# Optimization experiments

Measured on AMD Instinct MI355X. Metric: run time of the kernel, lower is better.

## Reference

```python
import jax, jax.numpy as jnp
import numpy as np

DIM = 256      # block dim
NH = 4         # num_head
HD = DIM // 2  # head_dim = dim // 2 (per CrossBlock -> CroA)
HALF = DIM // 2  # channels per axial branch
DI = NH * HD   # inner qkv dim = 512
B, H, W = 8, 56, 56


def _conv1x1(w, b, x):
    # 1x1 conv == per-pixel channel matmul; w:[Cout,Cin], x:[B,Cin,H,W]
    return jnp.einsum('oc,bchw->bohw', w, x) + b[None, :, None, None]


def _mha(x, qw, qb, kw, kb, vw, vb, pw, pb, rel):
    # axial MHA over the last (W) axis, per row, matching torch MHA exactly
    Bx, C, Hx, Wx = x.shape
    q = _conv1x1(qw, qb, x).transpose(0, 2, 1, 3).reshape(Bx, Hx, NH, HD, Wx)
    k = _conv1x1(kw, kb, x).transpose(0, 2, 1, 3).reshape(Bx, Hx, NH, HD, Wx)
    v = _conv1x1(vw, vb, x).transpose(0, 2, 1, 3).reshape(Bx, Hx, NH, HD, Wx)
    att = jnp.einsum('bhndi,bhndj->bhnij', q, k) * (HD ** -0.5)
    L = Wx
    # gathered relative-position bias (RelPos); torch does this under no_grad
    idx = (jnp.arange(L)[:, None] - jnp.arange(L)[None, :] + L - 1).reshape(-1)
    bias = jax.lax.stop_gradient(rel[:, idx].reshape(NH, L, L))
    att = jax.nn.softmax(att + bias[None, None], axis=-1)
    out = jnp.einsum('bhnij,bhndj->bhnid', att, v)  # [B,H,nh,W,hd]
    # faithful to torch: raw reshape of [B*H, nh, W, hd] -> (B, H, W, nh*hd)
    out = out.reshape(Bx, Hx, Wx, NH * HD).transpose(0, 3, 1, 2)
    return _conv1x1(pw, pb, out) + x


def _forward(x, xq_w, xq_b, xk_w, xk_b, xv_w, xv_b, xp_w, xp_b, rel_x,
             yq_w, yq_b, yk_w, yk_b, yv_w, yv_b, yp_w, yp_b, rel_y,
             cp_w, cp_b, m1_w, m1_b, m2_w, m2_b, ls1, ls2):
    ax, ay = jnp.split(x, 2, axis=1)
    ax = _mha(ax, xq_w, xq_b, xk_w, xk_b, xv_w, xv_b, xp_w, xp_b, rel_x)
    ay = _mha(ay.transpose(0, 1, 3, 2), yq_w, yq_b, yk_w, yk_b, yv_w, yv_b,
              yp_w, yp_b, rel_y).transpose(0, 1, 3, 2)
    net = _conv1x1(cp_w, cp_b, jnp.concatenate([ax, ay], axis=1))
    net = net * ls1[None] + x                      # layer_scale1 + residual
    h = jax.nn.gelu(_conv1x1(m1_w, m1_b, net), approximate=False)
    out = _conv1x1(m2_w, m2_b, h)
    return out * ls2[None] + net                   # layer_scale2 + identity skip (dim==out_dim)


def setup_inputs() -> dict:
    key = jax.random.key(0)
    ks = iter(jax.random.split(key, 32))
    def w(shape, s=0.05):
        return jax.random.normal(next(ks), shape, dtype=jnp.float32) * s
    return dict(
        x=jax.random.normal(next(ks), (B, DIM, H, W), dtype=jnp.float32),
        xq_w=w((DI, HALF)), xq_b=w((DI,)), xk_w=w((DI, HALF)), xk_b=w((DI,)),
        xv_w=w((DI, HALF)), xv_b=w((DI,)), xp_w=w((HALF, DI)), xp_b=w((HALF,)),
        rel_x=jax.random.normal(next(ks), (NH, W * W), dtype=jnp.float32),
        yq_w=w((DI, HALF)), yq_b=w((DI,)), yk_w=w((DI, HALF)), yk_b=w((DI,)),
        yv_w=w((DI, HALF)), yv_b=w((DI,)), yp_w=w((HALF, DI)), yp_b=w((HALF,)),
        rel_y=jax.random.normal(next(ks), (NH, H * H), dtype=jnp.float32),
        cp_w=w((DIM, DIM)), cp_b=w((DIM,)),
        m1_w=w((2 * DIM, DIM)), m1_b=w((2 * DIM,)),
        m2_w=w((DIM, 2 * DIM)), m2_b=w((DIM,)),
        ls1=jnp.ones((DIM, 1, 1), jnp.float32),
        ls2=jnp.ones((DIM, 1, 1), jnp.float32),
    )


def reference(x, xq_w, xq_b, xk_w, xk_b, xv_w, xv_b, xp_w, xp_b, rel_x,
              yq_w, yq_b, yk_w, yk_b, yv_w, yv_b, yp_w, yp_b, rel_y,
              cp_w, cp_b, m1_w, m1_b, m2_w, m2_b, ls1, ls2):
    return _forward(x, xq_w, xq_b, xk_w, xk_b, xv_w, xv_b, xp_w, xp_b, rel_x,
                    yq_w, yq_b, yk_w, yk_b, yv_w, yv_b, yp_w, yp_b, rel_y,
                    cp_w, cp_b, m1_w, m1_b, m2_w, m2_b, ls1, ls2)
```

## Files before the change

kernel.cpp:

```cpp
#include <hip/hip_runtime.h>

using u16 = unsigned short;
using u32 = unsigned int;

typedef short bf16x8 __attribute__((ext_vector_type(8)));
typedef float f32x4 __attribute__((ext_vector_type(4)));

#define HW 3136
#define IMG 56

__device__ __forceinline__ float bf2f(u16 v) {
    union { u32 u; float f; } c; c.u = ((u32)v) << 16; return c.f;
}
__device__ __forceinline__ u16 f2bf(float f) {
    union { float f; u32 u; } c; c.f = f;
    return (u16)((c.u + 0x7fffu + ((c.u >> 16) & 1u)) >> 16);
}
__device__ __forceinline__ u32 pk2bf(float a, float b) {
    u32 r;
    asm("v_cvt_pk_bf16_f32 %0, %1, %2" : "=v"(r) : "v"(a), "v"(b));
    return r;
}
__device__ __forceinline__ int swz8(int r) { return (r ^ (r >> 3)) & 7; }

__device__ __forceinline__ f32x4 mfma16(bf16x8 a, bf16x8 b, f32x4 c) {
    return __builtin_amdgcn_mfma_f32_16x16x32_bf16(a, b, c, 0, 0, 0);
}

__device__ __forceinline__ void gl_lds(const void* g, void* l) {
    __builtin_amdgcn_global_load_lds((const __attribute__((address_space(1))) void*)g,
                                     (__attribute__((address_space(3))) void*)l, 16, 0, 0);
}

__global__ __launch_bounds__(256) void prep(
    const float* __restrict__ x, u16* __restrict__ Xt,
    const float* __restrict__ s0, const float* __restrict__ s1, const float* __restrict__ s2,
    const float* __restrict__ s3, const float* __restrict__ s4, const float* __restrict__ s5,
    const float* __restrict__ s6, const float* __restrict__ s7, const float* __restrict__ s8,
    const float* __restrict__ s9, const float* __restrict__ s10,
    const float* __restrict__ b0, const float* __restrict__ b1, const float* __restrict__ b2,
    const float* __restrict__ b3, const float* __restrict__ b4, const float* __restrict__ b5,
    const float* __restrict__ b6, const float* __restrict__ b7, const float* __restrict__ b8,
    const float* __restrict__ b9, const float* __restrict__ b10,
    u16* __restrict__ Wb, float* __restrict__ Bc)
{
    __shared__ u16 lds[64][80];
    const int t = threadIdx.x;
    const int idx = blockIdx.x;

    if (idx < 1568) {
        const int Pb = (idx % 49) * 64;
        const int Cb = ((idx / 49) & 3) * 64;
        const int b  = idx / 196;
        #pragma unroll
        for (int q = 0; q < 4; ++q) {
            int id = t + q * 256;
            int c = id >> 4, pf = (id & 15) * 4;
            float4 v = *(const float4*)(x + ((long)(b * 256 + Cb + c)) * HW + Pb + pf);
            u16 vv[4] = { f2bf(v.x), f2bf(v.y), f2bf(v.z), f2bf(v.w) };
            #pragma unroll
            for (int j = 0; j < 4; ++j) {
                int p = pf + j;
                int cc = (((c >> 3) ^ ((p >> 2) & 7)) << 3) + (c & 7);
                lds[p][cc] = vv[j];
            }
        }
        __syncthreads();
        int p = t >> 2, cf = (t & 3) * 16;
        u16* dst = Xt + ((long)b * HW + Pb + p) * 256 + Cb + cf;
        int cc0 = ((cf >> 3) + 0) ^ ((p >> 2) & 7);
        int cc1 = ((cf >> 3) + 1) ^ ((p >> 2) & 7);
        *(uint4*)(dst + 0) = *(uint4*)&lds[p][cc0 * 8];
        *(uint4*)(dst + 8) = *(uint4*)&lds[p][cc1 * 8];
        return;
    }

    const int bx = idx - 1568;
    if (bx == 832) {
        for (int i = t; i < 4352; i += 256) {
            const float* src; int off;
            if      (i < 512)  { src = b0;  off = i; }
            else if (i < 1024) { src = b1;  off = i - 512; }
            else if (i < 1536) { src = b2;  off = i - 1024; }
            else if (i < 2048) { src = b3;  off = i - 1536; }
            else if (i < 2560) { src = b4;  off = i - 2048; }
            else if (i < 3072) { src = b5;  off = i - 2560; }
            else if (i < 3200) { src = b6;  off = i - 3072; }
            else if (i < 3328) { src = b7;  off = i - 3200; }
            else if (i < 3584) { src = b8;  off = i - 3328; }
            else if (i < 4096) { src = b9;  off = i - 3584; }
            else               { src = b10; off = i - 4096; }
            Bc[i] = src[off];
        }
        return;
    }
    long gid4 = ((long)bx * 256 + t) * 4;
    const float* src; long off;
    if (gid4 < 589824) {
        int seg = (int)(gid4 >> 16);
        const float* tab[9] = { s0, s1, s2, s3, s4, s5, s6, s7, s8 };
        src = tab[seg]; off = gid4 - ((long)seg << 16);
    } else if (gid4 < 720896) { src = s9;  off = gid4 - 589824; }
    else                      { src = s10; off = gid4 - 720896; }
    float4 v = *(const float4*)(src + off);
    *(uint2*)(Wb + gid4) = make_uint2(pk2bf(v.x, v.y), pk2bf(v.z, v.w));
}

__global__ __launch_bounds__(256, 2) void fused_attn(
    const u16* __restrict__ Wb, const float* __restrict__ Bc,
    const u16* __restrict__ Xt,
    const float* __restrict__ rel_x, const float* __restrict__ rel_y,
    u16* __restrict__ SbX, u16* __restrict__ SbY)
{
    __shared__ __align__(16) char smem[66048];
    const int tid = threadIdx.x;
    const int lane = tid & 63, wid = tid >> 6;
    const int l15 = lane & 15, lg = lane >> 4;

    const int g = blockIdx.x;
    const int n = blockIdx.y;
    const int branch = blockIdx.z >> 3;
    const int b = blockIdx.z & 7;

    const float* rel = branch ? rel_y : rel_x;
    u16* S = branch ? SbY : SbX;
    const u16* wsrc = Wb + branch * 196608 + n * 16384;
    const float* bsrc = Bc + branch * 1536 + n * 128;

    if (tid < 128) {
        float v = (tid < 112) ? rel[n * HW + tid] : 0.0f;
        *(float*)(smem + 65536 + tid * 4) = v;
    }

    bf16x8 wf[3][2][4];
    #pragma unroll
    for (int mat = 0; mat < 3; ++mat)
        #pragma unroll
        for (int mt = 0; mt < 2; ++mt) {
            int mrow = (wid * 2 + mt) * 16 + l15;
            const u16* wr = wsrc + mat * 65536 + mrow * 128;
            #pragma unroll
            for (int ks = 0; ks < 4; ++ks)
                wf[mat][mt][ks] = *(const bf16x8*)(wr + (ks * 4 + lg) * 8);
        }
    float4 bq4[2], bk4[2]; float bvv[2];
    #pragma unroll
    for (int mt = 0; mt < 2; ++mt) {
        int m0 = (wid * 2 + mt) * 16 + lg * 4;
        bq4[mt] = *(const float4*)(bsrc + m0);
        bk4[mt] = *(const float4*)(bsrc + 512 + m0);
        bvv[mt] = bsrc[1024 + (wid * 2 + mt) * 16 + l15];
    }

    const int istrip = wid * 16;
    const float qscale = 0.08838834764831845f;

    auto stageX = [&](int rc2) {
        const int i0 = wid * 16 + (lane >> 4);
        #pragma unroll
        for (int t = 0; t < 4; ++t) {
            int i = i0 + t * 4;
            int ic = (i > 55) ? 55 : i;
            long p = (branch == 0) ? (long)rc2 * IMG + ic : (long)ic * IMG + rc2;
            const u16* src = Xt + ((long)b * HW + p) * 256 + branch * 128
                             + (((lane & 15) ^ swz8(i)) * 8);
            gl_lds(src, smem + 49152 + wid * 4096 + t * 1024);
        }
    };

    stageX(g * 7);

    for (int r = 0; r < 7; ++r) {
        const int rc = g * 7 + r;

        __syncthreads();

        bf16x8 xf[4][4];
        #pragma unroll
        for (int it = 0; it < 4; ++it) {
            int i = it * 16 + l15;
            #pragma unroll
            for (int ks = 0; ks < 4; ++ks)
                xf[it][ks] = *(const bf16x8*)(smem + 49152 + i * 256
                                              + (((ks * 4 + lg) ^ swz8(i)) * 16));
        }

        __builtin_amdgcn_s_setprio(1);
        #pragma unroll
        for (int mat = 0; mat < 2; ++mat) {
            #pragma unroll
            for (int mt = 0; mt < 2; ++mt) {
                #pragma unroll
                for (int it = 0; it < 4; ++it) {
                    f32x4 a = {};
                    #pragma unroll
                    for (int ks = 0; ks < 4; ++ks)
                        a = mfma16(wf[mat][mt][ks], xf[it][ks], a);
                    int i = it * 16 + l15;
                    int m0 = (wid * 2 + mt) * 16 + lg * 4;
                    float4 bb2 = mat ? bk4[mt] : bq4[mt];
                    int c = m0 >> 3;
                    *(uint2*)(smem + mat * 16384 + i * 256 + ((c ^ swz8(i)) * 16) + (lg & 1) * 8)
                        = make_uint2(pk2bf(a[0] + bb2.x, a[1] + bb2.y),
                                     pk2bf(a[2] + bb2.z, a[3] + bb2.w));
                }
            }
        }
        #pragma unroll
        for (int mt = 0; mt < 2; ++mt) {
            #pragma unroll
            for (int it = 0; it < 4; ++it) {
                f32x4 a = {};
                #pragma unroll
                for (int ks = 0; ks < 4; ++ks)
                    a = mfma16(xf[it][ks], wf[2][mt][ks], a);
                int d = (wid * 2 + mt) * 16 + l15;
                int c2 = (it >> 1) * 4 + lg;
                float bv = bvv[mt];
                *(uint2*)(smem + 32768 + d * 128 + ((c2 ^ swz8(d)) * 16) + (it & 1) * 8)
                    = make_uint2(pk2bf(a[0] + bv, a[1] + bv),
                                 pk2bf(a[2] + bv, a[3] + bv));
            }
        }
        __builtin_amdgcn_s_setprio(0);
        __syncthreads();

        if (r < 6) stageX(rc + 1);

        bf16x8 aq[4];
        #pragma unroll
        for (int ks = 0; ks < 4; ++ks) {
            int row = istrip + l15;
            int ch = ks * 4 + lg;
            aq[ks] = *(const bf16x8*)(smem + row * 256 + ((ch ^ swz8(row)) * 16));
        }
        __builtin_amdgcn_s_setprio(1);
        f32x4 sacc[4] = {};
        #pragma unroll
        for (int ct = 0; ct < 4; ++ct) {
            #pragma unroll
            for (int ks = 0; ks < 4; ++ks) {
                int j = ct * 16 + l15;
                int ch = ks * 4 + lg;
                bf16x8 kb = *(const bf16x8*)(smem + 16384 + j * 256 + ((ch ^ swz8(j)) * 16));
                sacc[ct] = mfma16(kb, aq[ks], sacc[ct]);
            }
        }
        __builtin_amdgcn_s_setprio(0);

        const int irow = istrip + l15;
        float p[4][4];
        float mx = -1e30f;
        #pragma unroll
        for (int ct = 0; ct < 4; ++ct)
            #pragma unroll
            for (int rr = 0; rr < 4; ++rr) {
                int j = ct * 16 + lg * 4 + rr;
                float x = sacc[ct][rr] * qscale;
                if (j < IMG) x += *(const float*)(smem + 65536 + (irow - j + 55) * 4);
                else x = -1e30f;
                p[ct][rr] = x;
                mx = fmaxf(mx, x);
            }
        mx = fmaxf(mx, __shfl_xor(mx, 16));
        mx = fmaxf(mx, __shfl_xor(mx, 32));
        float s0 = 0.f;
        #pragma unroll
        for (int ct = 0; ct < 4; ++ct)
            #pragma unroll
            for (int rr = 0; rr < 4; ++rr) {
                float e = __expf(p[ct][rr] - mx);
                p[ct][rr] = e; s0 += e;
            }
        s0 += __shfl_xor(s0, 16);
        s0 += __shfl_xor(s0, 32);
        float inv = 1.0f / s0;

        union { u32 u[4]; bf16x8 v; } pb[2];
        #pragma unroll
        for (int ks = 0; ks < 2; ++ks) {
            pb[ks].u[0] = pk2bf(p[2*ks][0] * inv, p[2*ks][1] * inv);
            pb[ks].u[1] = pk2bf(p[2*ks][2] * inv, p[2*ks][3] * inv);
            pb[ks].u[2] = pk2bf(p[2*ks+1][0] * inv, p[2*ks+1][1] * inv);
            pb[ks].u[3] = pk2bf(p[2*ks+1][2] * inv, p[2*ks+1][3] * inv);
        }

        __builtin_amdgcn_s_setprio(1);
        f32x4 oacc[8] = {};
        #pragma unroll
        for (int dt = 0; dt < 8; ++dt) {
            #pragma unroll
            for (int ks = 0; ks < 2; ++ks) {
                int d = dt * 16 + l15;
                int c2 = ks * 4 + lg;
                bf16x8 vb = *(const bf16x8*)(smem + 32768 + d * 128 + ((c2 ^ swz8(d)) * 16));
                oacc[dt] = mfma16(vb, pb[ks].v, oacc[dt]);
            }
        }
        __builtin_amdgcn_s_setprio(0);

        const int i = istrip + l15;
        if (i < IMG) {
            int im = n * 14 + (i >> 2);
            long pp = (branch == 0) ? (long)rc * IMG + im : (long)im * IMG + rc;
            u16* dst = S + ((long)b * HW + pp) * 512 + (i & 3) * 128;
            #pragma unroll
            for (int dt = 0; dt < 8; ++dt) {
                int d4 = dt * 16 + lg * 4;
                *(uint2*)(dst + d4) = make_uint2(pk2bf(oacc[dt][0], oacc[dt][1]),
                                                 pk2bf(oacc[dt][2], oacc[dt][3]));
            }
        }
    }
}

__global__ __launch_bounds__(256, 2) void tail(
    const u16* __restrict__ Wb, const float* __restrict__ Bc,
    const u16* __restrict__ SbX, const u16* __restrict__ SbY,
    const u16* __restrict__ Xt,
    const float* __restrict__ ls1, const float* __restrict__ ls2,
    float* __restrict__ y)
{
    __shared__ __align__(16) char smem[81920];
    const int tid = threadIdx.x;
    const int lane = tid & 63, wid = tid >> 6;
    const int l15 = lane & 15, lg = lane >> 4;
    const int P0 = blockIdx.x * 64;
    const int b  = blockIdx.z;

    const u16* xp  = Wb + 393216;
    const u16* yp  = Wb + 458752;
    const u16* cpw = Wb + 524288;
    const u16* m1w = Wb + 589824;
    const u16* m2w = Wb + 720896;

    f32x4 acc[4][4] = {};
    for (int ko = 0; ko < 512; ko += 64) {
        #pragma unroll
        for (int t = 0; t < 2; ++t) {
            int row = wid * 16 + t * 8 + (lane >> 3);
            int c = (lane & 7) ^ swz8(row);
            long prow = (long)b * HW + P0 + row;
            gl_lds(SbX + prow * 512 + ko + c * 8, smem + wid * 2048 + t * 1024);
            gl_lds(SbY + prow * 512 + ko + c * 8, smem + 8192 + wid * 2048 + t * 1024);
        }
        #pragma unroll
        for (int t = 0; t < 4; ++t) {
            int row = wid * 32 + t * 8 + (lane >> 3);
            int c = (lane & 7) ^ swz8(row);
            gl_lds(xp + (long)row * 512 + ko + c * 8, smem + 16384 + wid * 4096 + t * 1024);
            gl_lds(yp + (long)row * 512 + ko + c * 8, smem + 32768 + wid * 4096 + t * 1024);
        }
        __syncthreads();

        const int actb = (wid < 2) ? 0 : 8192;
        const int wbse = (wid < 2) ? 16384 : 32768;
        const int wrow0 = (wid & 1) * 64;
        #pragma unroll
        for (int ks = 0; ks < 2; ++ks) {
            int ch = ks * 4 + lg;
            bf16x8 af[4], bfr[4];
            #pragma unroll
            for (int rt = 0; rt < 4; ++rt) {
                int row = rt * 16 + l15;
                af[rt] = *(const bf16x8*)(smem + actb + row * 128 + ((ch ^ swz8(row)) * 16));
            }
            #pragma unroll
            for (int ct = 0; ct < 4; ++ct) {
                int row = wrow0 + ct * 16 + l15;
                bfr[ct] = *(const bf16x8*)(smem + wbse + row * 128 + ((ch ^ swz8(row)) * 16));
            }
            #pragma unroll
            for (int rt = 0; rt < 4; ++rt)
                #pragma unroll
                for (int ct = 0; ct < 4; ++ct)
                    acc[rt][ct] = mfma16(bfr[ct], af[rt], acc[rt][ct]);
        }
        __syncthreads();
    }

    #pragma unroll
    for (int rt = 0; rt < 4; ++rt) {
        int pl = rt * 16 + l15;
        long rowp = (long)b * HW + P0 + pl;
        #pragma unroll
        for (int ct = 0; ct < 4; ++ct) {
            int mg2 = wid * 64 + ct * 16 + lg * 4;
            float4 bv = *(const float4*)(Bc + 3072 + mg2);
            ushort4 rv = *(const ushort4*)(Xt + rowp * 256 + mg2);
            float v0 = acc[rt][ct][0] + bv.x + bf2f(rv.x);
            float v1 = acc[rt][ct][1] + bv.y + bf2f(rv.y);
            float v2 = acc[rt][ct][2] + bv.z + bf2f(rv.z);
            float v3 = acc[rt][ct][3] + bv.w + bf2f(rv.w);
            int cc = mg2 >> 3;
            int pos = (cc & 24) | ((cc ^ swz8(pl)) & 7);
            *(uint2*)(smem + 49152 + pl * 512 + pos * 16 + (mg2 & 7) * 2)
                = make_uint2(pk2bf(v0, v1), pk2bf(v2, v3));
        }
    }
    __syncthreads();

    f32x4 acc2[4][4] = {};
    for (int ko = 0; ko < 256; ko += 64) {
        #pragma unroll
        for (int t = 0; t < 8; ++t) {
            int row = wid * 64 + t * 8 + (lane >> 3);
            int c = (lane & 7) ^ swz8(row);
            gl_lds(cpw + (long)row * 256 + ko + c * 8, smem + 16384 + wid * 8192 + t * 1024);
        }
        __syncthreads();

        #pragma unroll
        for (int ks = 0; ks < 2; ++ks) {
            int ch = ks * 4 + lg;
            bf16x8 af[4], bfr[4];
            #pragma unroll
            for (int rt = 0; rt < 4; ++rt) {
                int row = rt * 16 + l15;
                int c = (ko >> 3) + ch;
                int pos = (c & 24) | ((c ^ swz8(row)) & 7);
                af[rt] = *(const bf16x8*)(smem + 49152 + row * 512 + pos * 16);
            }
            #pragma unroll
            for (int ct = 0; ct < 4; ++ct) {
                int row = wid * 64 + ct * 16 + l15;
                bfr[ct] = *(const bf16x8*)(smem + 16384 + row * 128 + ((ch ^ swz8(row)) * 16));
            }
            #pragma unroll
            for (int rt = 0; rt < 4; ++rt)
                #pragma unroll
                for (int ct = 0; ct < 4; ++ct)
                    acc2[rt][ct] = mfma16(bfr[ct], af[rt], acc2[rt][ct]);
        }
        __syncthreads();
    }

    #pragma unroll
    for (int rt = 0; rt < 4; ++rt) {
        int pl = rt * 16 + l15;
        long rowp = (long)b * HW + P0 + pl;
        #pragma unroll
        for (int ct = 0; ct < 4; ++ct) {
            int mg = wid * 64 + ct * 16 + lg * 4;
            float4 bv = *(const float4*)(Bc + 3328 + mg);
            float4 sv = *(const float4*)(ls1 + mg);
            ushort4 rv = *(const ushort4*)(Xt + rowp * 256 + mg);
            float v0 = (acc2[rt][ct][0] + bv.x) * sv.x + bf2f(rv.x);
            float v1 = (acc2[rt][ct][1] + bv.y) * sv.y + bf2f(rv.y);
            float v2 = (acc2[rt][ct][2] + bv.z) * sv.z + bf2f(rv.z);
            float v3 = (acc2[rt][ct][3] + bv.w) * sv.w + bf2f(rv.w);
            int cc = mg >> 3;
            int pos = (cc & 24) | ((cc ^ swz8(pl)) & 7);
            *(uint2*)(smem + 16384 + pl * 512 + pos * 16 + (mg & 7) * 2)
                = make_uint2(pk2bf(v0, v1), pk2bf(v2, v3));
        }
    }

    f32x4 aco[4][4] = {};

    for (int hc = 0; hc < 4; ++hc) {
        f32x4 ach[4][2] = {};
        for (int ko = 0; ko < 256; ko += 64) {
            #pragma unroll
            for (int t = 0; t < 4; ++t) {
                int row = wid * 32 + t * 8 + (lane >> 3);
                int c = (lane & 7) ^ swz8(row);
                gl_lds(m1w + (long)(hc * 128 + row) * 256 + ko + c * 8,
                       smem + wid * 4096 + t * 1024);
            }
            __syncthreads();

            #pragma unroll
            for (int ks = 0; ks < 2; ++ks) {
                int ch = ks * 4 + lg;
                bf16x8 af[4], bfrh[2];
                #pragma unroll
                for (int rt = 0; rt < 4; ++rt) {
                    int row = rt * 16 + l15;
                    int c = (ko >> 3) + ch;
                    int pos = (c & 24) | ((c ^ swz8(row)) & 7);
                    af[rt] = *(const bf16x8*)(smem + 16384 + row * 512 + pos * 16);
                }
                #pragma unroll
                for (int mt = 0; mt < 2; ++mt) {
                    int row = wid * 32 + mt * 16 + l15;
                    bfrh[mt] = *(const bf16x8*)(smem + row * 128 + ((ch ^ swz8(row)) * 16));
                }
                #pragma unroll
                for (int rt = 0; rt < 4; ++rt)
                    #pragma unroll
                    for (int mt = 0; mt < 2; ++mt)
                        ach[rt][mt] = mfma16(bfrh[mt], af[rt], ach[rt][mt]);
            }
            __syncthreads();
        }
        #pragma unroll
        for (int rt = 0; rt < 4; ++rt) {
            int pl = rt * 16 + l15;
            #pragma unroll
            for (int mt = 0; mt < 2; ++mt) {
                int hloc = wid * 32 + mt * 16 + lg * 4;
                float4 bv = *(const float4*)(Bc + 3584 + hc * 128 + hloc);
                float v[4];
                #pragma unroll
                for (int j = 0; j < 4; ++j) {
                    float tt = ach[rt][mt][j] + ((const float*)&bv)[j];
                    v[j] = tt * 0.5f * (1.0f + erff(tt * 0.70710678118f));
                }
                int cc = hloc >> 3;
                int pos = (cc & 8) | ((cc ^ swz8(pl)) & 7);
                *(uint2*)(smem + 49152 + pl * 256 + pos * 16 + (hloc & 7) * 2)
                    = make_uint2(pk2bf(v[0], v[1]), pk2bf(v[2], v[3]));
            }
        }

        for (int ko = 0; ko < 128; ko += 64) {
            #pragma unroll
            for (int t = 0; t < 8; ++t) {
                int row = wid * 64 + t * 8 + (lane >> 3);
                int c = (lane & 7) ^ swz8(row);
                char* dst = ((wid < 2) ? (smem + wid * 8192) : (smem + 65536 + (wid - 2) * 8192))
                            + t * 1024;
                gl_lds(m2w + (long)row * 512 + hc * 128 + ko + c * 8, dst);
            }
            __syncthreads();

            #pragma unroll
            for (int ks = 0; ks < 2; ++ks) {
                int ch = ks * 4 + lg;
                bf16x8 af[4], bfr[4];
                #pragma unroll
                for (int rt = 0; rt < 4; ++rt) {
                    int row = rt * 16 + l15;
                    int c = (ko >> 3) + ch;
                    int pos = (c & 8) | ((c ^ swz8(row)) & 7);
                    af[rt] = *(const bf16x8*)(smem + 49152 + row * 256 + pos * 16);
                }
                #pragma unroll
                for (int ct = 0; ct < 4; ++ct) {
                    int row = wid * 64 + ct * 16 + l15;
                    const char* base = (wid < 2) ? smem : (smem + 65536 - 16384);
                    bfr[ct] = *(const bf16x8*)(base + row * 128 + ((ch ^ swz8(row)) * 16));
                }
                #pragma unroll
                for (int rt = 0; rt < 4; ++rt)
                    #pragma unroll
                    for (int ct = 0; ct < 4; ++ct)
                        aco[rt][ct] = mfma16(bfr[ct], af[rt], aco[rt][ct]);
            }
            __syncthreads();
        }
    }

    #pragma unroll
    for (int rt = 0; rt < 4; ++rt) {
        int pl = rt * 16 + l15;
        #pragma unroll
        for (int ct = 0; ct < 4; ++ct) {
            int mg = wid * 64 + ct * 16 + lg * 4;
            float4 bv = *(const float4*)(Bc + 4096 + mg);
            float4 sv = *(const float4*)(ls2 + mg);
            int cc = mg >> 3;
            int pos = (cc & 24) | ((cc ^ swz8(pl)) & 7);
            uint2 nv2 = *(const uint2*)(smem + 16384 + pl * 512 + pos * 16 + (mg & 7) * 2);
            u16 nv[4] = { (u16)(nv2.x & 0xffff), (u16)(nv2.x >> 16),
                          (u16)(nv2.y & 0xffff), (u16)(nv2.y >> 16) };
            aco[rt][ct][0] = (aco[rt][ct][0] + bv.x) * sv.x + bf2f(nv[0]);
            aco[rt][ct][1] = (aco[rt][ct][1] + bv.y) * sv.y + bf2f(nv[1]);
            aco[rt][ct][2] = (aco[rt][ct][2] + bv.z) * sv.z + bf2f(nv[2]);
            aco[rt][ct][3] = (aco[rt][ct][3] + bv.w) * sv.w + bf2f(nv[3]);
        }
    }
    __syncthreads();

    #pragma unroll
    for (int rt = 0; rt < 4; ++rt) {
        int pl = rt * 16 + l15;
        #pragma unroll
        for (int ct = 0; ct < 4; ++ct) {
            int mg = wid * 64 + ct * 16 + lg * 4;
            #pragma unroll
            for (int j = 0; j < 4; ++j)
                ((float*)smem)[(mg + j) * 65 + pl] = aco[rt][ct][j];
        }
    }
    __syncthreads();

    {
        const float* srcr = (const float*)smem + tid * 65;
        float* dst = y + ((long)(b * 256 + tid)) * HW + P0;
        #pragma unroll
        for (int k = 0; k < 16; ++k)
            *(float4*)(dst + k * 4) = *(const float4*)(srcr + k * 4);
    }
}

extern "C" void kernel_launch(void* const* d_in, const int* in_sizes, int n_in,
                              void* d_out, int out_size, void* d_ws, size_t ws_size,
                              hipStream_t stream)
{
    const float* x     = (const float*)d_in[0];
    const float* xq_w  = (const float*)d_in[1];
    const float* xq_b  = (const float*)d_in[2];
    const float* xk_w  = (const float*)d_in[3];
    const float* xk_b  = (const float*)d_in[4];
    const float* xv_w  = (const float*)d_in[5];
    const float* xv_b  = (const float*)d_in[6];
    const float* xp_w  = (const float*)d_in[7];
    const float* xp_b  = (const float*)d_in[8];
    const float* rel_x = (const float*)d_in[9];
    const float* yq_w  = (const float*)d_in[10];
    const float* yq_b  = (const float*)d_in[11];
    const float* yk_w  = (const float*)d_in[12];
    const float* yk_b  = (const float*)d_in[13];
    const float* yv_w  = (const float*)d_in[14];
    const float* yv_b  = (const float*)d_in[15];
    const float* yp_w  = (const float*)d_in[16];
    const float* yp_b  = (const float*)d_in[17];
    const float* rel_y = (const float*)d_in[18];
    const float* cp_w  = (const float*)d_in[19];
    const float* cp_b  = (const float*)d_in[20];
    const float* m1_w  = (const float*)d_in[21];
    const float* m1_b  = (const float*)d_in[22];
    const float* m2_w  = (const float*)d_in[23];
    const float* m2_b  = (const float*)d_in[24];
    const float* ls1   = (const float*)d_in[25];
    const float* ls2   = (const float*)d_in[26];

    if (ws_size < 128450560) return;

    char* ws = (char*)d_ws;
    u16*   SbY  = (u16*)(ws + 0);
    u16*   Wb   = (u16*)(ws + 25690112);
    float* Bc   = (float*)(ws + 27394048);
    u16*   Xt   = (u16*)(ws + 77070336);
    u16*   SbX  = (u16*)(ws + 89915392);

    dim3 blk(256, 1, 1);

    prep<<<dim3(2401, 1, 1), blk, 0, stream>>>(
        x, Xt,
        xq_w, xk_w, xv_w, yq_w, yk_w, yv_w, xp_w, yp_w, cp_w, m1_w, m2_w,
        xq_b, xk_b, xv_b, yq_b, yk_b, yv_b, xp_b, yp_b, cp_b, m1_b, m2_b,
        Wb, Bc);
    fused_attn<<<dim3(8, 4, 16), blk, 0, stream>>>(Wb, Bc, Xt, rel_x, rel_y, SbX, SbY);
    tail<<<dim3(49, 1, 8), blk, 0, stream>>>(Wb, Bc, SbX, SbY, Xt, ls1, ls2, (float*)d_out);
}
```

Before: 132.7 us.

## Double-buffer m1w weight tiles and raise wave priority around MFMA loops

The first MLP matmul now double-buffers its weight tiles between two LDS regions. The next K-slice is prefetched while MFMAs run on the current one, and the first slice of the next hidden chunk is prefetched after the second matmul finishes. This removes one barrier per K step and hides global-to-LDS load latency. s_setprio is raised around every MFMA inner loop so compute waves get scheduling preference. The cost is a second LDS buffer that shares space with the m2w staging area, which depends on careful barrier placement.

```diff
diff --git a/kernel.cpp b/kernel.cpp
--- a/kernel.cpp
+++ b/kernel.cpp
@@ -356,6 +356,7 @@
         const int actb = (wid < 2) ? 0 : 8192;
         const int wbse = (wid < 2) ? 16384 : 32768;
         const int wrow0 = (wid & 1) * 64;
+        __builtin_amdgcn_s_setprio(1);
         #pragma unroll
         for (int ks = 0; ks < 2; ++ks) {
             int ch = ks * 4 + lg;
@@ -376,6 +377,7 @@
                 for (int ct = 0; ct < 4; ++ct)
                     acc[rt][ct] = mfma16(bfr[ct], af[rt], acc[rt][ct]);
         }
+        __builtin_amdgcn_s_setprio(0);
         __syncthreads();
     }
 
@@ -410,6 +412,7 @@
         }
         __syncthreads();
 
+        __builtin_amdgcn_s_setprio(1);
         #pragma unroll
         for (int ks = 0; ks < 2; ++ks) {
             int ch = ks * 4 + lg;
@@ -432,6 +435,7 @@
                 for (int ct = 0; ct < 4; ++ct)
                     acc2[rt][ct] = mfma16(bfr[ct], af[rt], acc2[rt][ct]);
         }
+        __builtin_amdgcn_s_setprio(0);
         __syncthreads();
     }
 
@@ -458,18 +462,31 @@
 
     f32x4 aco[4][4] = {};
 
+    #pragma unroll
+    for (int t = 0; t < 4; ++t) {
+        int row = wid * 32 + t * 8 + (lane >> 3);
+        int c = (lane & 7) ^ swz8(row);
+        gl_lds(m1w + (long)row * 256 + c * 8, smem + wid * 4096 + t * 1024);
+    }
+
     for (int hc = 0; hc < 4; ++hc) {
         f32x4 ach[4][2] = {};
-        for (int ko = 0; ko < 256; ko += 64) {
-            #pragma unroll
-            for (int t = 0; t < 4; ++t) {
-                int row = wid * 32 + t * 8 + (lane >> 3);
-                int c = (lane & 7) ^ swz8(row);
-                gl_lds(m1w + (long)(hc * 128 + row) * 256 + ko + c * 8,
-                       smem + wid * 4096 + t * 1024);
-            }
+        #pragma unroll
+        for (int idx = 0; idx < 4; ++idx) {
             __syncthreads();
-
+            if (idx < 3) {
+                char* nbuf = ((idx & 1) == 0) ? (smem + 65536) : smem;
+                #pragma unroll
+                for (int t = 0; t < 4; ++t) {
+                    int row = wid * 32 + t * 8 + (lane >> 3);
+                    int c = (lane & 7) ^ swz8(row);
+                    gl_lds(m1w + (long)(hc * 128 + row) * 256 + (idx + 1) * 64 + c * 8,
+                           nbuf + wid * 4096 + t * 1024);
+                }
+            }
+            const char* cbuf = ((idx & 1) == 0) ? smem : (smem + 65536);
+            const int ko = idx * 64;
+            __builtin_amdgcn_s_setprio(1);
             #pragma unroll
             for (int ks = 0; ks < 2; ++ks) {
                 int ch = ks * 4 + lg;
@@ -484,7 +501,7 @@
                 #pragma unroll
                 for (int mt = 0; mt < 2; ++mt) {
                     int row = wid * 32 + mt * 16 + l15;
-                    bfrh[mt] = *(const bf16x8*)(smem + row * 128 + ((ch ^ swz8(row)) * 16));
+                    bfrh[mt] = *(const bf16x8*)(cbuf + row * 128 + ((ch ^ swz8(row)) * 16));
                 }
                 #pragma unroll
                 for (int rt = 0; rt < 4; ++rt)
@@ -492,8 +509,9 @@
                     for (int mt = 0; mt < 2; ++mt)
                         ach[rt][mt] = mfma16(bfrh[mt], af[rt], ach[rt][mt]);
             }
-            __syncthreads();
-        }
+            __builtin_amdgcn_s_setprio(0);
+        }
+
         #pragma unroll
         for (int rt = 0; rt < 4; ++rt) {
             int pl = rt * 16 + l15;
@@ -513,6 +531,7 @@
                     = make_uint2(pk2bf(v[0], v[1]), pk2bf(v[2], v[3]));
             }
         }
+        __syncthreads();
 
         for (int ko = 0; ko < 128; ko += 64) {
             #pragma unroll
@@ -525,6 +544,7 @@
             }
             __syncthreads();
 
+            __builtin_amdgcn_s_setprio(1);
             #pragma unroll
             for (int ks = 0; ks < 2; ++ks) {
                 int ch = ks * 4 + lg;
@@ -548,7 +568,18 @@
                     for (int ct = 0; ct < 4; ++ct)
                         aco[rt][ct] = mfma16(bfr[ct], af[rt], aco[rt][ct]);
             }
+            __builtin_amdgcn_s_setprio(0);
             __syncthreads();
+        }
+
+        if (hc < 3) {
+            #pragma unroll
+            for (int t = 0; t < 4; ++t) {
+                int row = wid * 32 + t * 8 + (lane >> 3);
+                int c = (lane & 7) ^ swz8(row);
+                gl_lds(m1w + (long)((hc + 1) * 128 + row) * 256 + c * 8,
+                       smem + wid * 4096 + t * 1024);
+            }
         }
     }
 
```

Measured after the change: 132.0 us (median of 3 runs). About the same (-0.5%).
